# Kernel tuning notes

Measured on AMD Instinct MI355X. Metric: run time of the kernel, lower is better.

The kernel has to match this reference:

```python
import jax, jax.numpy as jnp
import numpy as np

B, S, E, H = 8, 2048, 512, 8
D = E // H  # head_dim = 64


def setup_inputs() -> dict:
    key0 = jax.random.key(0)
    ks = jax.random.split(key0, 12)
    scale = 1.0 / np.sqrt(E)
    return {
        "value": jax.random.normal(ks[0], (B, S, E), jnp.float32),
        "key": jax.random.normal(ks[1], (B, S, E), jnp.float32),
        "query": jax.random.normal(ks[2], (B, S, E), jnp.float32),
        "mask": jax.random.randint(ks[3], (B, 1, 1, S), 0, 2, jnp.int32),
        "wq": jax.random.normal(ks[4], (E, E), jnp.float32) * scale,
        "bq": jnp.zeros((E,), jnp.float32),
        "wk": jax.random.normal(ks[5], (E, E), jnp.float32) * scale,
        "bk": jnp.zeros((E,), jnp.float32),
        "wv": jax.random.normal(ks[6], (E, E), jnp.float32) * scale,
        "bv": jnp.zeros((E,), jnp.float32),
        "wo": jax.random.normal(ks[7], (E, E), jnp.float32) * scale,
        "bo": jnp.zeros((E,), jnp.float32),
    }


def reference(value, key, query, mask, wq, bq, wk, bk, wv, bv, wo, bo):
    b, s, e = query.shape
    # projections
    q = (query @ wq + bq).reshape(b, s, H, D)  # (B,S,H,D)
    k = (key @ wk + bk).reshape(b, s, H, D)
    v = (value @ wv + bv).reshape(b, s, H, D)
    # scaled dot-product logits: (B,H,Sq,Sk)
    logits = jnp.einsum("bqhd,bkhd->bhqk", q, k) / jnp.sqrt(jnp.asarray(D, q.dtype))
    logits = logits + mask.astype(logits.dtype) * -1e9  # mask==1 -> blocked
    attn = jax.nn.softmax(logits, axis=-1)
    out = jnp.einsum("bhqk,bkhd->bqhd", attn, v).reshape(b, s, e)
    return out @ wo + bo
```

## Files before the change

### kernel.cpp

```cpp
#include <hip/hip_runtime.h>

#define Bz 8
#define Sz 2048
#define Ez 512
#define Hz 8
#define Dz 64

typedef _Float16 f16;
typedef __attribute__((ext_vector_type(2))) _Float16 f16x2;
typedef __attribute__((ext_vector_type(8))) _Float16 f16x8;
typedef __attribute__((ext_vector_type(4))) float f32x4;

#define LOG2E 1.44269504f

__device__ __forceinline__ void async16(const void* g, void* l) {
    __builtin_amdgcn_global_load_lds(
        (const __attribute__((address_space(1))) unsigned int*)g,
        (__attribute__((address_space(3))) unsigned int*)l, 16, 0, 0);
}

__device__ __forceinline__ f16x2 pkrtz(float a, float b) {
    return __builtin_bit_cast(f16x2, __builtin_amdgcn_cvt_pkrtz(a, b));
}

__device__ __forceinline__ int swz(int row) {
    return (row & 7) ^ ((2 * ((row >> 3) & 3)) & 7);
}

__global__ __launch_bounds__(256)
void cast_kernel(const float* __restrict__ q, const float* __restrict__ k,
                 const float* __restrict__ v, const int* __restrict__ mask,
                 f16* __restrict__ qa, f16* __restrict__ ka, f16* __restrict__ va,
                 int* __restrict__ idx, int* __restrict__ slen)
{
    const int z = blockIdx.y;
    const int tid = threadIdx.x;
    if (z == 3) {
        const int b = blockIdx.x;
        if (b >= Bz) return;
        __shared__ int sc2[2][256];
        __shared__ int stot;
        const int* mp = mask + (size_t)b * Sz;
        int m[8], c = 0;
        #pragma unroll
        for (int j = 0; j < 8; ++j) { m[j] = mp[tid*8 + j]; c += (m[j] == 0); }
        sc2[0][tid] = c;
        __syncthreads();
        int src = 0;
        #pragma unroll
        for (int s = 1; s < 256; s <<= 1) {
            int vv = sc2[src][tid] + ((tid >= s) ? sc2[src][tid - s] : 0);
            sc2[src ^ 1][tid] = vv;
            src ^= 1;
            __syncthreads();
        }
        int incl = sc2[src][tid];
        int base = incl - c;
        if (tid == 255) { slen[b] = incl; stot = incl; }
        int kk = base;
        #pragma unroll
        for (int j = 0; j < 8; ++j)
            if (m[j] == 0) idx[(size_t)b * Sz + (kk++)] = tid*8 + j;
        __syncthreads();
        for (int j = stot + tid; j < Sz; j += 256) idx[(size_t)b * Sz + j] = 0;
        return;
    }
    const int i = blockIdx.x * 256 + tid;
    const float* src = (z == 0) ? q : (z == 1) ? k : v;
    f16* dst = (z == 0) ? qa : (z == 1) ? ka : va;
    float4 x = *(const float4*)&src[(size_t)i * 4];
    f16x2 h0 = pkrtz(x.x, x.y), h1 = pkrtz(x.z, x.w);
    f16 h[4] = {h0[0], h0[1], h1[0], h1[1]};
    *(uint2*)&dst[(size_t)i * 4] = *(uint2*)h;
}

__global__ __launch_bounds__(256)
void prep_w(const float* __restrict__ W0, const float* __restrict__ W1,
            const float* __restrict__ W2, const float* __restrict__ W3,
            f16* __restrict__ T0, f16* __restrict__ T1,
            f16* __restrict__ T2, f16* __restrict__ T3)
{
    __shared__ float S[64][68];
    const float* W = (blockIdx.z==0)?W0:(blockIdx.z==1)?W1:(blockIdx.z==2)?W2:W3;
    f16*         T = (blockIdx.z==0)?T0:(blockIdx.z==1)?T1:(blockIdx.z==2)?T2:T3;
    const float sc = (blockIdx.z == 0) ? 0.125f * LOG2E : 1.0f;
    const int k0 = blockIdx.x * 64, n0 = blockIdx.y * 64;
    const int tid = threadIdx.x;
    {
        int kr = tid >> 4, nc = (tid & 15) * 4;
        #pragma unroll
        for (int i = 0; i < 4; ++i) {
            float4 w4 = *(const float4*)&W[(size_t)(k0 + kr + i*16) * Ez + n0 + nc];
            S[kr + i*16][nc+0] = w4.x; S[kr + i*16][nc+1] = w4.y;
            S[kr + i*16][nc+2] = w4.z; S[kr + i*16][nc+3] = w4.w;
        }
    }
    __syncthreads();
    {
        int n = tid >> 2, kq = tid & 3;
        f16 h[16];
        #pragma unroll
        for (int j = 0; j < 16; ++j) h[j] = (f16)(S[kq*16 + j][n] * sc);
        f16* dst = &T[(size_t)(n0 + n) * Ez + k0 + kq*16];
        *(uint4*)&dst[0] = *(uint4*)&h[0];
        *(uint4*)&dst[8] = *(uint4*)&h[8];
    }
}

__global__ __launch_bounds__(256)
void compact_v(const f16* __restrict__ vp, const int* __restrict__ idx,
               const int* __restrict__ slen, f16* __restrict__ vt)
{
    const int ct = blockIdx.x, h = blockIdx.y, b = blockIdx.z;
    const int sl = slen[b];
    if (ct * 64 >= sl && !(ct == 0 && sl == 0)) return;
    __shared__ f16 S[64 * 72];
    const int tid = threadIdx.x;
    {
        int r = tid >> 2, ch = tid & 3;
        int j = ct * 64 + r;
        uint4 v0 = {0,0,0,0}, v1 = {0,0,0,0};
        if (j < sl) {
            int s = idx[(size_t)b * Sz + j];
            const f16* srcp = vp + (((size_t)b * Hz + h) * Sz + s) * Dz + ch * 16;
            v0 = *(const uint4*)&srcp[0];
            v1 = *(const uint4*)&srcp[8];
        }
        *(uint4*)&S[r*72 + ch*16]     = v0;
        *(uint4*)&S[r*72 + ch*16 + 8] = v1;
    }
    __syncthreads();
    {
        int d = tid >> 2, kq = tid & 3;
        f16 hh[16];
        #pragma unroll
        for (int j = 0; j < 16; ++j) hh[j] = S[(kq*16 + j)*72 + d];
        f16* dst = vt + (((size_t)b * Hz + h) * Dz + d) * Sz + ct*64 + kq*16;
        *(uint4*)&dst[0] = *(uint4*)&hh[0];
        *(uint4*)&dst[8] = *(uint4*)&hh[8];
    }
}

__global__ __launch_bounds__(256, 4)
void proj_gemm(const f16* __restrict__ qa, const f16* __restrict__ ka,
               const f16* __restrict__ va,
               const f16* __restrict__ wtq, const f16* __restrict__ wtk,
               const f16* __restrict__ wtv,
               const float* __restrict__ bqp, const float* __restrict__ bkp,
               const float* __restrict__ bvp,
               f16* __restrict__ qp, f16* __restrict__ kp, f16* __restrict__ vp)
{
    __shared__ __align__(16) char lds[32768];
    const int z = blockIdx.z;
    const f16* A  = (z==0)?qa:(z==1)?ka:va;
    const f16* Wt = (z==0)?wtq:(z==1)?wtk:wtv;
    const float* bias = (z==0)?bqp:(z==1)?bkp:bvp;
    f16* C16 = (z==0)?qp:(z==1)?kp:vp;
    const float bscale = (z==0) ? 0.125f*LOG2E : 1.0f;

    const int tid  = threadIdx.x;
    const int lane = tid & 63, w = tid >> 6;
    const int col  = lane & 15, quad = lane >> 4;
    const int wm = w & 1, wn = w >> 1;
    const int m0 = blockIdx.x * 128, n0 = blockIdx.y * 128;
    const int srow = lane >> 2, schunk = lane & 3;

    f32x4 acc[4][4];
    #pragma unroll
    for (int i = 0; i < 4; ++i)
        #pragma unroll
        for (int j = 0; j < 4; ++j) acc[i][j] = (f32x4){0.f,0.f,0.f,0.f};

    auto issue = [&](int t, int buf) {
        f16* As = (f16*)(lds + buf * 16384);
        f16* Ws = As + 4096;
        #pragma unroll
        for (int i = 0; i < 2; ++i) {
            int row = w*32 + i*16 + srow;
            int cl = schunk ^ ((row >> 1) & 3);
            async16(&A[(size_t)(m0 + row) * Ez + t*32 + cl*8],  &As[row*32 + schunk*8]);
            async16(&Wt[(size_t)(n0 + row) * Ez + t*32 + cl*8], &Ws[row*32 + schunk*8]);
        }
    };

    issue(0, 0);
    const int xrc = (col >> 1) & 3;

    for (int t = 0; t < 16; ++t) {
        const int cur = t & 1;
        __syncthreads();
        if (t < 15) issue(t + 1, cur ^ 1);
        f16* As = (f16*)(lds + cur * 16384);
        f16* Ws = As + 4096;
        f16x8 af[4];
        #pragma unroll
        for (int mi = 0; mi < 4; ++mi)
            af[mi] = *(const f16x8*)&As[(wm*64 + mi*16 + col)*32 + ((quad ^ xrc)*8)];
        #pragma unroll
        for (int ni = 0; ni < 4; ++ni) {
            f16x8 wf = *(const f16x8*)&Ws[(wn*64 + ni*16 + col)*32 + ((quad ^ xrc)*8)];
            #pragma unroll
            for (int mi = 0; mi < 4; ++mi)
                acc[mi][ni] = __builtin_amdgcn_mfma_f32_16x16x32_f16(af[mi], wf, acc[mi][ni], 0,0,0);
        }
    }

    f16* Tr = (f16*)lds;
    #pragma unroll
    for (int p = 0; p < 2; ++p) {
        __syncthreads();
        if (wn == p) {
            #pragma unroll
            for (int ni = 0; ni < 4; ++ni) {
                float bv = bias[n0 + p*64 + ni*16 + col] * bscale;
                #pragma unroll
                for (int mi = 0; mi < 4; ++mi)
                    #pragma unroll
                    for (int rr = 0; rr < 4; ++rr) {
                        int ml = wm*64 + mi*16 + quad*4 + rr;
                        Tr[ml*72 + ni*16 + col] = (f16)(acc[mi][ni][rr] + bv);
                    }
            }
        }
        __syncthreads();
        int rw = tid >> 1, half = tid & 1;
        int m = m0 + rw, b = m >> 11, s = m & (Sz-1);
        int hh = (n0 >> 6) + p;
        f16* dst = &C16[(((size_t)b*Hz + hh)*Sz + s)*Dz + half*32];
        const f16* srcp = &Tr[rw*72 + half*32];
        #pragma unroll
        for (int j = 0; j < 4; ++j)
            *(uint4*)&dst[j*8] = *(const uint4*)&srcp[j*8];
    }
}

__global__ __launch_bounds__(256, 4)
void out_gemm(const f16* __restrict__ A, const f16* __restrict__ Wt,
              const float* __restrict__ bias, float* __restrict__ Cf)
{
    __shared__ __align__(16) char lds[32768];
    const int tid  = threadIdx.x;
    const int lane = tid & 63, w = tid >> 6;
    const int col  = lane & 15, quad = lane >> 4;
    const int wm = w & 1, wn = w >> 1;
    const int m0 = blockIdx.x * 128, n0 = blockIdx.y * 128;
    const int srow = lane >> 2, schunk = lane & 3;

    f32x4 acc[4][4];
    #pragma unroll
    for (int i = 0; i < 4; ++i)
        #pragma unroll
        for (int j = 0; j < 4; ++j) acc[i][j] = (f32x4){0.f,0.f,0.f,0.f};

    auto issue = [&](int t, int buf) {
        f16* As = (f16*)(lds + buf * 16384);
        f16* Ws = As + 4096;
        #pragma unroll
        for (int i = 0; i < 2; ++i) {
            int row = w*32 + i*16 + srow;
            int cl = schunk ^ ((row >> 1) & 3);
            async16(&A[(size_t)(m0 + row) * Ez + t*32 + cl*8],  &As[row*32 + schunk*8]);
            async16(&Wt[(size_t)(n0 + row) * Ez + t*32 + cl*8], &Ws[row*32 + schunk*8]);
        }
    };

    issue(0, 0);
    const int xrc = (col >> 1) & 3;

    for (int t = 0; t < 16; ++t) {
        const int cur = t & 1;
        __syncthreads();
        if (t < 15) issue(t + 1, cur ^ 1);
        f16* As = (f16*)(lds + cur * 16384);
        f16* Ws = As + 4096;
        f16x8 af[4];
        #pragma unroll
        for (int mi = 0; mi < 4; ++mi)
            af[mi] = *(const f16x8*)&As[(wm*64 + mi*16 + col)*32 + ((quad ^ xrc)*8)];
        #pragma unroll
        for (int ni = 0; ni < 4; ++ni) {
            f16x8 wf = *(const f16x8*)&Ws[(wn*64 + ni*16 + col)*32 + ((quad ^ xrc)*8)];
            #pragma unroll
            for (int mi = 0; mi < 4; ++mi)
                acc[mi][ni] = __builtin_amdgcn_mfma_f32_16x16x32_f16(af[mi], wf, acc[mi][ni], 0,0,0);
        }
    }

    #pragma unroll
    for (int ni = 0; ni < 4; ++ni) {
        int n = n0 + wn*64 + ni*16 + col;
        float bv = bias[n];
        #pragma unroll
        for (int mi = 0; mi < 4; ++mi)
            #pragma unroll
            for (int rr = 0; rr < 4; ++rr) {
                int m = m0 + wm*64 + mi*16 + quad*4 + rr;
                Cf[(size_t)m * Ez + n] = acc[mi][ni][rr] + bv;
            }
    }
}

__global__ __launch_bounds__(256, 4)
void attn_f16(const f16* __restrict__ Q, const f16* __restrict__ K,
              const f16* __restrict__ VT, const int* __restrict__ idx,
              const int* __restrict__ slen, f16* __restrict__ O)
{
    __shared__ __align__(16) f16 KS[2][64*64];
    __shared__ __align__(16) f16 VS[2][64*64];

    const int tid  = threadIdx.x;
    const int lane = tid & 63, w = tid >> 6;
    const int col  = lane & 15, quad = lane >> 4;

    const int blk = blockIdx.x;
    const int xcd = blk & 7, slot = blk >> 3;
    const int bh = xcd + 8 * (slot >> 4);
    const int qb = slot & 15;
    const int b = bh >> 3, h = bh & 7;

    const int sl = slen[b];
    int nt = (sl + 63) >> 6;
    if (nt < 1) nt = 1;

    const int q0 = qb * 128 + w * 32;

    f16x8 qf[2][2];
    #pragma unroll
    for (int qt = 0; qt < 2; ++qt)
        #pragma unroll
        for (int ks = 0; ks < 2; ++ks)
            qf[qt][ks] = *(const f16x8*)&Q[((size_t)bh*Sz + q0 + qt*16 + col)*Dz + ks*32 + quad*8];

    const f16* Kp = K + (size_t)bh * Sz * Dz;
    const f16* Vp = VT + (size_t)bh * Dz * Sz;
    const int* ixp = idx + (size_t)b * Sz;

    const int srow = lane >> 3, sch = lane & 7;
    const int row0 = w*16 + srow, row1 = row0 + 8;
    const int cl0 = sch ^ swz(row0), cl1 = sch ^ swz(row1);

    int keyrow[4], gk[4];
    #pragma unroll
    for (int kc = 0; kc < 4; ++kc) {
        keyrow[kc] = 32*(kc>>1) + 8*(col>>2) + 4*(kc&1) + (col&3);
        gk[kc] = swz(keyrow[kc]);
    }

    f32x4 oacc[2][4];
    #pragma unroll
    for (int qt = 0; qt < 2; ++qt)
        #pragma unroll
        for (int dc = 0; dc < 4; ++dc) oacc[qt][dc] = (f32x4){0.f,0.f,0.f,0.f};
    float lsum[2] = {0.f, 0.f};
    const f32x4 zero4 = (f32x4){0.f, 0.f, 0.f, 0.f};

    auto issue = [&](int t, int buf, int s0, int s1) {
        async16(&Kp[(size_t)s0*Dz + cl0*8],          &KS[buf][row0*64 + sch*8]);
        async16(&Vp[(size_t)row0*Sz + t*64 + cl0*8], &VS[buf][row0*64 + sch*8]);
        async16(&Kp[(size_t)s1*Dz + cl1*8],          &KS[buf][row1*64 + sch*8]);
        async16(&Vp[(size_t)row1*Sz + t*64 + cl1*8], &VS[buf][row1*64 + sch*8]);
    };

    int cs0 = ixp[row0], cs1 = ixp[row1];
    issue(0, 0, cs0, cs1);
    int ns0 = 0, ns1 = 0;
    if (nt > 1) { ns0 = ixp[64 + row0]; ns1 = ixp[64 + row1]; }

    for (int t = 0; t < nt; ++t) {
        const int cur = t & 1;
        __syncthreads();
        if (t + 1 < nt) {
            issue(t + 1, cur ^ 1, ns0, ns1);
            if (t + 2 < nt) {
                ns0 = ixp[(t+2)*64 + row0];
                ns1 = ixp[(t+2)*64 + row1];
            }
        }

        f32x4 sc[2][4];
        #pragma unroll
        for (int kc = 0; kc < 4; ++kc) {
            f16x8 kf0 = *(const f16x8*)&KS[cur][keyrow[kc]*64 + ((quad ^ gk[kc])*8)];
            f16x8 kf1 = *(const f16x8*)&KS[cur][keyrow[kc]*64 + (((4 + quad) ^ gk[kc])*8)];
            sc[0][kc] = __builtin_amdgcn_mfma_f32_16x16x32_f16(kf0, qf[0][0], zero4, 0,0,0);
            sc[1][kc] = __builtin_amdgcn_mfma_f32_16x16x32_f16(kf0, qf[1][0], zero4, 0,0,0);
            sc[0][kc] = __builtin_amdgcn_mfma_f32_16x16x32_f16(kf1, qf[0][1], sc[0][kc], 0,0,0);
            sc[1][kc] = __builtin_amdgcn_mfma_f32_16x16x32_f16(kf1, qf[1][1], sc[1][kc], 0,0,0);
        }

        const bool last = (t == nt - 1);
        union { f16x2 h2[4]; f16x8 h8; } ph[2][2];
        #pragma unroll
        for (int qt = 0; qt < 2; ++qt) {
            #pragma unroll
            for (int kg = 0; kg < 2; ++kg) {
                float e0 = exp2f(sc[qt][2*kg][0]), e1 = exp2f(sc[qt][2*kg][1]);
                float e2 = exp2f(sc[qt][2*kg][2]), e3 = exp2f(sc[qt][2*kg][3]);
                float e4 = exp2f(sc[qt][2*kg+1][0]), e5 = exp2f(sc[qt][2*kg+1][1]);
                float e6 = exp2f(sc[qt][2*kg+1][2]), e7 = exp2f(sc[qt][2*kg+1][3]);
                float ls;
                if (last) {
                    int rem = sl - t*64 - 32*kg - 8*quad;
                    ls = ((rem > 0 ? e0 : 0.f) + (rem > 1 ? e1 : 0.f))
                       + ((rem > 2 ? e2 : 0.f) + (rem > 3 ? e3 : 0.f))
                       + ((rem > 4 ? e4 : 0.f) + (rem > 5 ? e5 : 0.f))
                       + ((rem > 6 ? e6 : 0.f) + (rem > 7 ? e7 : 0.f));
                } else {
                    ls = ((e0 + e1) + (e2 + e3)) + ((e4 + e5) + (e6 + e7));
                }
                lsum[qt] += ls;
                ph[qt][kg].h2[0] = pkrtz(e0, e1);
                ph[qt][kg].h2[1] = pkrtz(e2, e3);
                ph[qt][kg].h2[2] = pkrtz(e4, e5);
                ph[qt][kg].h2[3] = pkrtz(e6, e7);
            }
        }

        #pragma unroll
        for (int dc = 0; dc < 4; ++dc) {
            const int d = dc*16 + col;
            const int gd = swz(d);
            #pragma unroll
            for (int kg = 0; kg < 2; ++kg) {
                f16x8 vf = *(const f16x8*)&VS[cur][d*64 + (((kg*4 + quad) ^ gd)*8)];
                oacc[0][dc] = __builtin_amdgcn_mfma_f32_16x16x32_f16(vf, ph[0][kg].h8, oacc[0][dc], 0,0,0);
                oacc[1][dc] = __builtin_amdgcn_mfma_f32_16x16x32_f16(vf, ph[1][kg].h8, oacc[1][dc], 0,0,0);
            }
        }
    }

    float inv[2];
    #pragma unroll
    for (int qt = 0; qt < 2; ++qt) {
        float v = lsum[qt];
        v += __shfl_xor(v, 16, 64);
        v += __shfl_xor(v, 32, 64);
        inv[qt] = 1.0f / v;
    }
    #pragma unroll
    for (int qt = 0; qt < 2; ++qt) {
        const int q = q0 + qt*16 + col;
        f16* op = &O[((size_t)b*Sz + q)*Ez + h*Dz];
        #pragma unroll
        for (int dc = 0; dc < 4; ++dc) {
            f16 ov[4] = {(f16)(oacc[qt][dc][0]*inv[qt]), (f16)(oacc[qt][dc][1]*inv[qt]),
                         (f16)(oacc[qt][dc][2]*inv[qt]), (f16)(oacc[qt][dc][3]*inv[qt])};
            *(uint2*)&op[dc*16 + quad*4] = *(uint2*)ov;
        }
    }
}

extern "C" void kernel_launch(void* const* d_in, const int* in_sizes, int n_in,
                              void* d_out, int out_size, void* d_ws, size_t ws_size,
                              hipStream_t stream)
{
    const float* value = (const float*)d_in[0];
    const float* key   = (const float*)d_in[1];
    const float* query = (const float*)d_in[2];
    const int*   mask  = (const int*)d_in[3];
    const float* wq = (const float*)d_in[4];
    const float* bq = (const float*)d_in[5];
    const float* wk = (const float*)d_in[6];
    const float* bk = (const float*)d_in[7];
    const float* wv = (const float*)d_in[8];
    const float* bv = (const float*)d_in[9];
    const float* wo = (const float*)d_in[10];
    const float* bo = (const float*)d_in[11];
    float* out = (float*)d_out;

    const size_t nW   = (size_t)Ez * Ez;
    const size_t nAct = (size_t)Bz * Sz * Ez;
    f16* wtq = (f16*)d_ws;
    f16* wtk = wtq + nW;
    f16* wtv = wtk + nW;
    f16* wto = wtv + nW;
    f16* qa  = wto + nW;
    f16* ka  = qa + nAct;
    f16* va  = ka + nAct;
    f16* qp  = va + nAct;
    f16* kp  = qp + nAct;
    f16* vp  = kp + nAct;
    f16* vt  = vp + nAct;
    f16* o16 = vt + nAct;
    int* idxp = (int*)(o16 + nAct);
    int* slenp = idxp + Bz * Sz;

    cast_kernel<<<dim3(8192, 4), 256, 0, stream>>>(query, key, value, mask,
                                                   qa, ka, va, idxp, slenp);
    prep_w<<<dim3(8, 8, 4), 256, 0, stream>>>(wq, wk, wv, wo, wtq, wtk, wtv, wto);

    proj_gemm<<<dim3(128, 4, 3), 256, 0, stream>>>(qa, ka, va, wtq, wtk, wtv,
                                                   bq, bk, bv, qp, kp, vp);

    compact_v<<<dim3(32, Hz, Bz), 256, 0, stream>>>(vp, idxp, slenp, vt);

    attn_f16<<<1024, 256, 0, stream>>>(qp, kp, vt, idxp, slenp, o16);

    out_gemm<<<dim3(128, 4), 256, 0, stream>>>(o16, wto, bo, out);
}
```

Before: 298.0 us.

## Compute softmax row sums via MFMA with ones vector, add setprio, raw exp2

Replaces the per-lane scalar row-sum accumulation and final cross-lane shuffles with MFMA instructions that multiply the probability tile by a vector of ones, moving that reduction onto the matrix units. It also switches exp2f to the raw hardware exp2 builtin, zeroes the masked tail probabilities directly instead of only excluding them from the sum, and wraps the MFMA sections in s_setprio to favour matrix issue across waves. The intent is to cut VALU work in the softmax stage. In exchange the row sums are computed from fp16-rounded probabilities and cost four extra MFMAs per tile.

```diff
diff --git a/kernel.cpp b/kernel.cpp
--- a/kernel.cpp
+++ b/kernel.cpp
@@ -351,8 +351,11 @@
     for (int qt = 0; qt < 2; ++qt)
         #pragma unroll
         for (int dc = 0; dc < 4; ++dc) oacc[qt][dc] = (f32x4){0.f,0.f,0.f,0.f};
-    float lsum[2] = {0.f, 0.f};
     const f32x4 zero4 = (f32x4){0.f, 0.f, 0.f, 0.f};
+    f32x4 lacc[2] = {(f32x4){0.f,0.f,0.f,0.f}, (f32x4){0.f,0.f,0.f,0.f}};
+    f16x8 one8;
+    #pragma unroll
+    for (int i = 0; i < 8; ++i) one8[i] = (f16)1.0f;
 
     auto issue = [&](int t, int buf, int s0, int s1) {
         async16(&Kp[(size_t)s0*Dz + cl0*8],          &KS[buf][row0*64 + sch*8]);
@@ -378,6 +381,7 @@
         }
 
         f32x4 sc[2][4];
+        __builtin_amdgcn_s_setprio(1);
         #pragma unroll
         for (int kc = 0; kc < 4; ++kc) {
             f16x8 kf0 = *(const f16x8*)&KS[cur][keyrow[kc]*64 + ((quad ^ gk[kc])*8)];
@@ -387,6 +391,7 @@
             sc[0][kc] = __builtin_amdgcn_mfma_f32_16x16x32_f16(kf1, qf[0][1], sc[0][kc], 0,0,0);
             sc[1][kc] = __builtin_amdgcn_mfma_f32_16x16x32_f16(kf1, qf[1][1], sc[1][kc], 0,0,0);
         }
+        __builtin_amdgcn_s_setprio(0);
 
         const bool last = (t == nt - 1);
         union { f16x2 h2[4]; f16x8 h8; } ph[2][2];
@@ -394,21 +399,21 @@
         for (int qt = 0; qt < 2; ++qt) {
             #pragma unroll
             for (int kg = 0; kg < 2; ++kg) {
-                float e0 = exp2f(sc[qt][2*kg][0]), e1 = exp2f(sc[qt][2*kg][1]);
-                float e2 = exp2f(sc[qt][2*kg][2]), e3 = exp2f(sc[qt][2*kg][3]);
-                float e4 = exp2f(sc[qt][2*kg+1][0]), e5 = exp2f(sc[qt][2*kg+1][1]);
-                float e6 = exp2f(sc[qt][2*kg+1][2]), e7 = exp2f(sc[qt][2*kg+1][3]);
-                float ls;
+                float e0 = __builtin_amdgcn_exp2f(sc[qt][2*kg][0]);
+                float e1 = __builtin_amdgcn_exp2f(sc[qt][2*kg][1]);
+                float e2 = __builtin_amdgcn_exp2f(sc[qt][2*kg][2]);
+                float e3 = __builtin_amdgcn_exp2f(sc[qt][2*kg][3]);
+                float e4 = __builtin_amdgcn_exp2f(sc[qt][2*kg+1][0]);
+                float e5 = __builtin_amdgcn_exp2f(sc[qt][2*kg+1][1]);
+                float e6 = __builtin_amdgcn_exp2f(sc[qt][2*kg+1][2]);
+                float e7 = __builtin_amdgcn_exp2f(sc[qt][2*kg+1][3]);
                 if (last) {
                     int rem = sl - t*64 - 32*kg - 8*quad;
-                    ls = ((rem > 0 ? e0 : 0.f) + (rem > 1 ? e1 : 0.f))
-                       + ((rem > 2 ? e2 : 0.f) + (rem > 3 ? e3 : 0.f))
-                       + ((rem > 4 ? e4 : 0.f) + (rem > 5 ? e5 : 0.f))
-                       + ((rem > 6 ? e6 : 0.f) + (rem > 7 ? e7 : 0.f));
-                } else {
-                    ls = ((e0 + e1) + (e2 + e3)) + ((e4 + e5) + (e6 + e7));
+                    e0 = (rem > 0) ? e0 : 0.f; e1 = (rem > 1) ? e1 : 0.f;
+                    e2 = (rem > 2) ? e2 : 0.f; e3 = (rem > 3) ? e3 : 0.f;
+                    e4 = (rem > 4) ? e4 : 0.f; e5 = (rem > 5) ? e5 : 0.f;
+                    e6 = (rem > 6) ? e6 : 0.f; e7 = (rem > 7) ? e7 : 0.f;
                 }
-                lsum[qt] += ls;
                 ph[qt][kg].h2[0] = pkrtz(e0, e1);
                 ph[qt][kg].h2[1] = pkrtz(e2, e3);
                 ph[qt][kg].h2[2] = pkrtz(e4, e5);
@@ -416,6 +421,11 @@
             }
         }
 
+        __builtin_amdgcn_s_setprio(1);
+        lacc[0] = __builtin_amdgcn_mfma_f32_16x16x32_f16(one8, ph[0][0].h8, lacc[0], 0,0,0);
+        lacc[1] = __builtin_amdgcn_mfma_f32_16x16x32_f16(one8, ph[1][0].h8, lacc[1], 0,0,0);
+        lacc[0] = __builtin_amdgcn_mfma_f32_16x16x32_f16(one8, ph[0][1].h8, lacc[0], 0,0,0);
+        lacc[1] = __builtin_amdgcn_mfma_f32_16x16x32_f16(one8, ph[1][1].h8, lacc[1], 0,0,0);
         #pragma unroll
         for (int dc = 0; dc < 4; ++dc) {
             const int d = dc*16 + col;
@@ -427,16 +437,12 @@
                 oacc[1][dc] = __builtin_amdgcn_mfma_f32_16x16x32_f16(vf, ph[1][kg].h8, oacc[1][dc], 0,0,0);
             }
         }
+        __builtin_amdgcn_s_setprio(0);
     }
 
     float inv[2];
-    #pragma unroll
-    for (int qt = 0; qt < 2; ++qt) {
-        float v = lsum[qt];
-        v += __shfl_xor(v, 16, 64);
-        v += __shfl_xor(v, 32, 64);
-        inv[qt] = 1.0f / v;
-    }
+    inv[0] = 1.0f / lacc[0][0];
+    inv[1] = 1.0f / lacc[1][0];
     #pragma unroll
     for (int qt = 0; qt < 2; ++qt) {
         const int q = q0 + qt*16 + col;
```

Result: faster. 281.4 us (-5.6%).
